# Kernel optimization log

Hardware: AMD Instinct MI355X
Metric: run time of the kernel (lower is better)

## Reference

```python
import jax, jax.numpy as jnp
import numpy as np

B, N, T_FULL, T, KS, FEAT = 32, 360, 512, 64, 8, 8
NLAYERS = 3   # DCGRU layers
GLAYERS = 4   # bidirectional GRU layers in GruKRegion


def _gru_layer(x, Wih, Whh, bih, bhh, reverse):
    # x: [M, Tg, in] -> [M, Tg, H]; PyTorch GRU gate order (r, z, n)
    M = x.shape[0]
    Hh = Whh.shape[1]
    xp = jnp.einsum('mti,gi->mtg', x, Wih) + bih  # precompute input projections
    if reverse:
        xp = xp[:, ::-1]

    def step(h, xg):
        gh = jnp.einsum('mh,gh->mg', h, Whh) + bhh
        xr, xz, xn = jnp.split(xg, 3, -1)
        hr, hz, hn = jnp.split(gh, 3, -1)
        r = jax.nn.sigmoid(xr + hr)
        z = jax.nn.sigmoid(xz + hz)
        n = jnp.tanh(xn + r * hn)
        hnew = (1.0 - z) * n + z * h
        return hnew, hnew

    _, hs = jax.lax.scan(step, jnp.zeros((M, Hh), x.dtype), jnp.swapaxes(xp, 0, 1))
    hs = jnp.swapaxes(hs, 0, 1)
    if reverse:
        hs = hs[:, ::-1]
    return hs


def _dcgru_cell(x, h, adj, gw, gb, cw, cb):
    # x, h: [B, N] (rnn_units = 1); adj: [B, N, N]; max_diffusion_step = 2
    def gconv(inp, st, W, bias):
        x0 = jnp.stack([inp, st], axis=-1)                     # [B,N,2]
        x1 = jnp.einsum('bnm,bmc->bnc', adj, x0)
        x2 = 2.0 * jnp.einsum('bnm,bmc->bnc', adj, x1) - x0    # Chebyshev recurrence
        # torch layout: [B,N,C,num_matrices] flattened channel-major
        xc = jnp.stack([x0, x1, x2], axis=-1).reshape(x0.shape[0], N, 6)
        return jnp.einsum('bnf,fo->bno', xc, W) + bias

    gates = jax.nn.sigmoid(gconv(x, h, gw, gb))                # [B,N,2]
    r, u = gates[..., 0], gates[..., 1]
    c = jnp.tanh(gconv(x, r * h, cw, cb)[..., 0])
    return u * h + (1.0 - u) * c


def _forward(full_seq, reconstruct_seq, node_feas, temperature,
             g0wih, g0whh, g0bih, g0bhh, gwih, gwhh, gbih, gbhh,
             l1w, l1b, l2w, l2b,
             enc_gw, enc_gb, enc_cw, enc_cb,
             dec_gw, dec_gb, dec_cw, dec_cb, proj_w, proj_b):
    b, n, tfull = full_seq.shape
    # ---- GruKRegion feature extractor ----
    x = full_seq.reshape(b * n, tfull // KS, KS)
    out = jnp.concatenate(
        [_gru_layer(x, g0wih[0], g0whh[0], g0bih[0], g0bhh[0], False),
         _gru_layer(x, g0wih[1], g0whh[1], g0bih[1], g0bhh[1], True)], axis=-1)
    for l in range(GLAYERS - 1):
        out = jnp.concatenate(
            [_gru_layer(out, gwih[l, 0], gwhh[l, 0], gbih[l, 0], gbhh[l, 0], False),
             _gru_layer(out, gwih[l, 1], gwhh[l, 1], gbih[l, 1], gbhh[l, 1], True)], axis=-1)
    feat = out[:, -1, :].reshape(b, n, 2 * KS)
    feat = jax.nn.leaky_relu(jnp.einsum('bnf,of->bno', feat, l1w) + l1b, 0.2)
    feat = jnp.einsum('bnf,of->bno', feat, l2w) + l2b          # [B,N,FEAT]
    # ---- Embed2GraphByProduct ----
    logits = jnp.einsum('bjk,bpk->bjp', feat, feat)            # [B,N,N]
    # ---- hard gumbel softmax ----
    U = jax.random.uniform(jax.random.key(42), logits.shape, logits.dtype)
    g = -jnp.log(-jnp.log(U + 1e-10) + 1e-10)
    y_soft = jax.nn.softmax((logits + g) / temperature, axis=-1)
    y_hard = jax.nn.one_hot(jnp.argmax(y_soft, -1), n, dtype=y_soft.dtype)
    adj = y_soft + jax.lax.stop_gradient(y_hard - y_soft)
    adj = jnp.where(jnp.eye(n, dtype=bool), 0.0, adj)          # zero diagonal
    # (original computes a random-walk matrix then discards it; skipped)
    # ---- encoder: scan over time, 3 stacked DCGRU layers ----
    seq = jnp.transpose(reconstruct_seq, (2, 0, 1))            # [T,B,N]

    def enc_step(hid, xt):
        o = xt
        new = []
        for l in range(NLAYERS):
            hnew = _dcgru_cell(o, hid[l], adj, enc_gw[l], enc_gb[l], enc_cw[l], enc_cb[l])
            new.append(hnew)
            o = hnew
        return jnp.stack(new), None

    hid, _ = jax.lax.scan(enc_step, jnp.zeros((NLAYERS, b, n), seq.dtype), seq)

    def dec_step(carry, _):
        hidc, inp = carry
        o = inp
        new = []
        for l in range(NLAYERS):
            hnew = _dcgru_cell(o, hidc[l], adj, dec_gw[l], dec_gb[l], dec_cw[l], dec_cb[l])
            new.append(hnew)
            o = hnew
        proj = o * proj_w[0, 0] + proj_b[0]                    # Linear(1,1)
        return (jnp.stack(new), proj), proj

    _, outs = jax.lax.scan(dec_step, (hid, jnp.zeros((b, n), seq.dtype)), None, length=T)
    return jnp.transpose(outs, (1, 2, 0))                      # [B,N,T]


def setup_inputs():
    key = jax.random.key(0)
    ks = jax.random.split(key, 24)
    s = 0.2
    p = lambda k, sh: jax.random.normal(k, sh, jnp.float32) * s
    return dict(
        full_seq=jax.random.normal(ks[0], (B, N, T_FULL), jnp.float32),
        reconstruct_seq=jax.random.normal(ks[1], (B, N, T), jnp.float32),
        node_feas=jax.random.normal(ks[2], (B, N, KS), jnp.float32),
        temperature=jnp.ones((), jnp.float32),
        g0wih=p(ks[3], (2, 3 * KS, KS)), g0whh=p(ks[4], (2, 3 * KS, KS)),
        g0bih=p(ks[5], (2, 3 * KS)), g0bhh=p(ks[6], (2, 3 * KS)),
        gwih=p(ks[7], (GLAYERS - 1, 2, 3 * KS, 2 * KS)),
        gwhh=p(ks[8], (GLAYERS - 1, 2, 3 * KS, KS)),
        gbih=p(ks[9], (GLAYERS - 1, 2, 3 * KS)), gbhh=p(ks[10], (GLAYERS - 1, 2, 3 * KS)),
        l1w=p(ks[11], (KS, 2 * KS)), l1b=p(ks[12], (KS,)),
        l2w=p(ks[13], (FEAT, KS)), l2b=p(ks[14], (FEAT,)),
        enc_gw=p(ks[15], (NLAYERS, 6, 2)), enc_gb=jnp.ones((NLAYERS, 2), jnp.float32),
        enc_cw=p(ks[16], (NLAYERS, 6, 1)), enc_cb=jnp.zeros((NLAYERS, 1), jnp.float32),
        dec_gw=p(ks[17], (NLAYERS, 6, 2)), dec_gb=jnp.ones((NLAYERS, 2), jnp.float32),
        dec_cw=p(ks[18], (NLAYERS, 6, 1)), dec_cb=jnp.zeros((NLAYERS, 1), jnp.float32),
        proj_w=p(ks[19], (1, 1)), proj_b=jnp.zeros((1,), jnp.float32),
    )


def reference(full_seq, reconstruct_seq, node_feas, temperature,
              g0wih, g0whh, g0bih, g0bhh, gwih, gwhh, gbih, gbhh,
              l1w, l1b, l2w, l2b,
              enc_gw, enc_gb, enc_cw, enc_cb,
              dec_gw, dec_gb, dec_cw, dec_cb, proj_w, proj_b):
    return _forward(full_seq, reconstruct_seq, node_feas, temperature,
                    g0wih, g0whh, g0bih, g0bhh, gwih, gwhh, gbih, gbhh,
                    l1w, l1b, l2w, l2b,
                    enc_gw, enc_gb, enc_cw, enc_cb,
                    dec_gw, dec_gb, dec_cw, dec_cb, proj_w, proj_b)
```

## Files before the change

kernel.cpp:

```cpp
#include <hip/hip_runtime.h>
#include <math.h>

#define M_SEQ 11520
#define NNODE 360
#define NB    32
#define TT    64

__device__ __forceinline__ float fsigd(float x)  { return 1.0f / (1.0f + __expf(-x)); }
__device__ __forceinline__ float ftanhd(float x) { return 1.0f - 2.0f / (__expf(2.0f * x) + 1.0f); }

__device__ __forceinline__ void lds_barrier()
{
    asm volatile("s_waitcnt lgkmcnt(0)" ::: "memory");
    __builtin_amdgcn_sched_barrier(0);
    __builtin_amdgcn_s_barrier();
    __builtin_amdgcn_sched_barrier(0);
}

__device__ __forceinline__ unsigned rotl32(unsigned x, int n) { return (x << n) | (x >> (32 - n)); }

__device__ __forceinline__ void tf2x32(unsigned& x0, unsigned& x1)
{
    const unsigned k0 = 0u, k1 = 42u, k2 = 0u ^ 42u ^ 0x1BD11BDAu;
    x0 += k0; x1 += k1;
#define R4(a,b,c,d) \
    x0 += x1; x1 = rotl32(x1,a); x1 ^= x0; \
    x0 += x1; x1 = rotl32(x1,b); x1 ^= x0; \
    x0 += x1; x1 = rotl32(x1,c); x1 ^= x0; \
    x0 += x1; x1 = rotl32(x1,d); x1 ^= x0;
    R4(13,15,26,6)   x0 += k1; x1 += k2 + 1u;
    R4(17,29,16,24)  x0 += k2; x1 += k0 + 2u;
    R4(13,15,26,6)   x0 += k0; x1 += k1 + 3u;
    R4(17,29,16,24)  x0 += k1; x1 += k2 + 4u;
    R4(13,15,26,6)   x0 += k2; x1 += k0 + 5u;
#undef R4
}

__device__ __forceinline__ float jax_uniform(unsigned idx)
{
    unsigned x0 = 0u, x1 = idx;
    tf2x32(x0, x1);
    unsigned bits = x0 ^ x1;
    return __uint_as_float((bits >> 9) | 0x3f800000u) - 1.0f;
}

template<int K>
__device__ __forceinline__ void swz_gather(float h, float* __restrict__ hb)
{
    hb[K] = __int_as_float(
        __builtin_amdgcn_ds_swizzle(__float_as_int(h), (K << 5) | 0x18));
    if constexpr (K < 7)
        swz_gather<K + 1>(h, hb);
}

template<int I>
__device__ __forceinline__ void ldx(float* __restrict__ xv, const float* __restrict__ p)
{
    const float4* p4 = reinterpret_cast<const float4*>(p);
#pragma unroll
    for (int q = 0; q < I / 4; ++q) {
        float4 f = p4[q];
        xv[4*q] = f.x; xv[4*q+1] = f.y; xv[4*q+2] = f.z; xv[4*q+3] = f.w;
    }
}

template<int I>
__device__ __forceinline__ void xgates(const float* __restrict__ xv,
    const float* wx0, const float* wx1, const float* wx2,
    float bx0, float bx1, float bx2, float& xr, float& xz, float& xn)
{
    xr = bx0; xz = bx1; xn = bx2;
#pragma unroll
    for (int k = 0; k < I; ++k) {
        xr += xv[k] * wx0[k];
        xz += xv[k] * wx1[k];
        xn += xv[k] * wx2[k];
    }
}

__device__ __forceinline__ float hstep(float h, float xr, float xz, float xn,
    const float* w0, const float* w1, const float* w2,
    float bh0, float bh1, float bh2)
{
    float hb[8];
    swz_gather<0>(h, hb);
    float gh0 = bh0, gh1 = bh1, gh2 = bh2;
#pragma unroll
    for (int k = 0; k < 8; ++k) {
        gh0 += hb[k] * w0[k];
        gh1 += hb[k] * w1[k];
        gh2 += hb[k] * w2[k];
    }
    float r  = fsigd(xr + gh0);
    float z  = fsigd(xz + gh1);
    float nn = ftanhd(xn + r * gh2);
    return (1.f - z) * nn + z * h;
}

template<int I, bool LASTONLY>
__global__ __launch_bounds__(256) void gru_fused(
    const float* __restrict__ x,
    const float* __restrict__ wih,
    const float* __restrict__ whh,
    const float* __restrict__ bih,
    const float* __restrict__ bhh,
    float* __restrict__ out)
{
    const int tid = blockIdx.x * 256 + threadIdx.x;
    const int j   = tid & 7;
    const int md  = tid >> 3;
    if (md >= M_SEQ * 2) return;
    const int m = md >> 1, dir = md & 1;

    float wx0[I], wx1[I], wx2[I];
    const float* WI = wih + dir * 24 * I;
#pragma unroll
    for (int k = 0; k < I; ++k) {
        wx0[k] = WI[j * I + k];
        wx1[k] = WI[(8 + j) * I + k];
        wx2[k] = WI[(16 + j) * I + k];
    }
    float w0[8], w1[8], w2[8];
    const float* WH = whh + dir * 192;
#pragma unroll
    for (int k = 0; k < 8; ++k) {
        w0[k] = WH[j * 8 + k];
        w1[k] = WH[(8 + j) * 8 + k];
        w2[k] = WH[(16 + j) * 8 + k];
    }
    const float bx0 = bih[dir*24 + j], bx1 = bih[dir*24 + 8 + j], bx2 = bih[dir*24 + 16 + j];
    const float bh0 = bhh[dir*24 + j], bh1 = bhh[dir*24 + 8 + j], bh2 = bhh[dir*24 + 16 + j];

    const float* xm = x + (size_t)m * TT * I;
    float* om = out + (size_t)m * TT * 16 + dir * 8 + j;

    const int tstep = dir ? -1 : 1;
    const int tbase = dir ? TT - 1 : 0;

    float h = 0.f;
    float xva[I], xvb[I];
    ldx<I>(xva, xm + (tbase) * I);
    ldx<I>(xvb, xm + (tbase + tstep) * I);
    float cr, cz, cn;
    xgates<I>(xva, wx0, wx1, wx2, bx0, bx1, bx2, cr, cz, cn);

    for (int tt = 0; tt < TT; tt += 2) {
        const int t0 = tbase + tstep * tt;
        const int t1 = t0 + tstep;
        if (tt + 2 < TT) ldx<I>(xva, xm + (t0 + 2 * tstep) * I);
        float nr, nz, nn;
        xgates<I>(xvb, wx0, wx1, wx2, bx0, bx1, bx2, nr, nz, nn);
        h = hstep(h, cr, cz, cn, w0, w1, w2, bh0, bh1, bh2);
        if (!LASTONLY || t0 == TT - 1) om[t0 * 16] = h;
        if (tt + 3 < TT) ldx<I>(xvb, xm + (t0 + 3 * tstep) * I);
        h = hstep(h, nr, nz, nn, w0, w1, w2, bh0, bh1, bh2);
        if (!LASTONLY || t1 == TT - 1) om[t1 * 16] = h;
        xgates<I>(xva, wx0, wx1, wx2, bx0, bx1, bx2, cr, cz, cn);
    }
}

__global__ void feat_kernel(const float* __restrict__ gout,
                            const float* __restrict__ l1w, const float* __restrict__ l1b,
                            const float* __restrict__ l2w, const float* __restrict__ l2b,
                            float* __restrict__ feat)
{
    int m = blockIdx.x * blockDim.x + threadIdx.x;
    if (m >= M_SEQ) return;
    const float* xp = gout + (size_t)m * TT * 16 + (TT - 1) * 16;
    float xv[16];
#pragma unroll
    for (int i = 0; i < 16; ++i) xv[i] = xp[i];
    float h1[8];
#pragma unroll
    for (int o = 0; o < 8; ++o) {
        float a = 0.f;
#pragma unroll
        for (int f = 0; f < 16; ++f) a += xv[f] * l1w[o * 16 + f];
        a += l1b[o];
        h1[o] = (a >= 0.f) ? a : 0.2f * a;
    }
#pragma unroll
    for (int o = 0; o < 8; ++o) {
        float a = 0.f;
#pragma unroll
        for (int f = 0; f < 8; ++f) a += h1[f] * l2w[o * 8 + f];
        feat[(size_t)m * 8 + o] = a + l2b[o];
    }
}

__global__ void adj_kernel(const float* __restrict__ feat,
                           const float* __restrict__ tptr,
                           int* __restrict__ colp, float* __restrict__ vp)
{
    const int gw   = (blockIdx.x * blockDim.x + threadIdx.x) >> 6;
    const int lane = threadIdx.x & 63;
    if (gw >= NB * NNODE) return;
    const int b = gw / NNODE;
    const int n = gw - b * NNODE;
    const float T = tptr[0];
    const float* fb = feat + (size_t)b * NNODE * 8;
    float fn[8];
#pragma unroll
    for (int k = 0; k < 8; ++k) fn[k] = fb[(size_t)n * 8 + k];

    float sv[6];
    float mval = -3.0e38f; int midx = 1 << 30;
#pragma unroll
    for (int s = 0; s < 6; ++s) {
        int p = s * 64 + lane;
        float xs = -3.0e38f;
        if (p < NNODE) {
            const float* fp = fb + (size_t)p * 8;
            float d = 0.f;
#pragma unroll
            for (int k = 0; k < 8; ++k) d += fn[k] * fp[k];
            unsigned idx = (unsigned)gw * 360u + (unsigned)p;
            float u   = jax_uniform(idx);
            float gum = -logf(-logf(u + 1e-10f) + 1e-10f);
            xs = (d + gum) / T;
            if (xs > mval) { mval = xs; midx = p; }
        }
        sv[s] = xs;
    }
    for (int off = 32; off > 0; off >>= 1) {
        float ov = __shfl_xor(mval, off);
        int   oi = __shfl_xor(midx, off);
        if (ov > mval || (ov == mval && oi < midx)) { mval = ov; midx = oi; }
    }
    float ssum = 0.f;
#pragma unroll
    for (int s = 0; s < 6; ++s) {
        int p = s * 64 + lane;
        if (p < NNODE) ssum += expf(sv[s] - mval);
    }
    for (int off = 32; off > 0; off >>= 1) ssum += __shfl_xor(ssum, off);
    if (lane == 0) {
        float ys = 1.0f / ssum;
        float v  = ys + (1.0f - ys);
        if (midx == n) v = 0.0f;
        colp[gw] = midx;
        vp[gw]   = v;
    }
}

__device__ __forceinline__ void dc_layer(
    bool comp,
    float o_own, float oa, float ob,
    float& hn, float ha, float hb,
    float v, float vv, int c1, int c2, bool act, int n,
    const float* __restrict__ W, float bgr, float bgu,
    const float* __restrict__ C, float cb,
    float* __restrict__ s_rh)
{
    float f1 = 0.f, f2 = 0.f, f4 = 0.f, f5 = 0.f, rh = 0.f;
    if (comp) {
        f1 = v * oa; f2 = vv * ob - o_own;
        f4 = v * ha; f5 = vv * hb - hn;
        float r = fsigd(o_own*W[0] + f1*W[2] + f2*W[4] + hn*W[6] + f4*W[8] + f5*W[10] + bgr);
        rh = r * hn;
        if (act) s_rh[n] = rh;
    }
    lds_barrier();
    if (comp) {
        float rha = s_rh[c1], rhb = s_rh[c2];
        float u  = fsigd(o_own*W[1] + f1*W[3] + f2*W[5] + hn*W[7] + f4*W[9] + f5*W[11] + bgu);
        float cnd = ftanhd(o_own*C[0] + f1*C[1] + f2*C[2] + rh*C[3]
                           + (v*rha)*C[4] + (vv*rhb - rh)*C[5] + cb);
        hn = u * hn + (1.f - u) * cnd;
    }
}

__global__ __launch_bounds__(768, 1) void decode_kernel(
    const float* __restrict__ rec,
    const int*   __restrict__ colp, const float* __restrict__ vp,
    const float* __restrict__ egw, const float* __restrict__ egb,
    const float* __restrict__ ecw, const float* __restrict__ ecb,
    const float* __restrict__ dgw, const float* __restrict__ dgb,
    const float* __restrict__ dcw, const float* __restrict__ dcb,
    const float* __restrict__ pw,  const float* __restrict__ pb,
    float* __restrict__ outp)
{
    __shared__ float s_h[2][3][NNODE];
    __shared__ float s_xe[2][NNODE];
    __shared__ float s_r1[2][NNODE];
    __shared__ float s_u1[2][NNODE];
    __shared__ float s_c1[2][NNODE];
    __shared__ float s_rh0[NNODE];
    __shared__ float s_rh2[NNODE];
    __shared__ float s_o[NNODE];
    __shared__ float s_rhd[NNODE];
    __shared__ float s_v[NNODE];
    __shared__ int   s_c[NNODE];

    const int  b    = blockIdx.x;
    const int  tid  = threadIdx.x;
    const bool isB  = tid >= 384;
    const bool isA  = !isB;
    const int  node = isB ? tid - 384 : tid;
    const bool actN = node < NNODE;

    const float* recb = rec + ((size_t)b * NNODE + node) * TT;

    float o_own = 0.f, xq1 = 0.f;
    if (isA && actN) {
        s_c[node] = colp[b * NNODE + node];
        s_v[node] = vp[b * NNODE + node];
        o_own = recb[0];
        xq1   = recb[1];
        s_xe[0][node] = o_own;
#pragma unroll
        for (int l = 0; l < 3; ++l) { s_h[0][l][node] = 0.f; s_h[1][l][node] = 0.f; }
    }
    __syncthreads();

    int c1 = 0, c2 = 0;
    float v = 0.f, vv = 0.f;
    if (actN) {
        c1 = s_c[node];
        c2 = s_c[c1];
        v  = s_v[node];
        vv = 2.f * v * s_v[c1];
    }
    const float projw = pw[0], projb = pb[0];

    float Wg[36], Bg[6], Wc[18], Cb[3];
#pragma unroll
    for (int k = 0; k < 36; ++k) Wg[k] = egw[k];
#pragma unroll
    for (int k = 0; k < 6;  ++k) Bg[k] = egb[k];
#pragma unroll
    for (int k = 0; k < 18; ++k) Wc[k] = ecw[k];
#pragma unroll
    for (int k = 0; k < 3;  ++k) Cb[k] = ecb[k];

    float h0r = 0.f, h1r = 0.f, h2r = 0.f;

    for (int k = 0; k <= TT; ++k) {
        const int  pk = k & 1, qk = pk ^ 1;
        const bool aAct = isA && actN && (k < TT);
        const bool bAct = isB && actN && (k >= 1);
        float nx2 = 0.f;
        if (aAct && k + 2 < TT) nx2 = recb[k + 2];

        float fA1=0.f, fA2=0.f, fA4=0.f, fA5=0.f, rhA=0.f;
        if (isA) {
            float xa  = s_xe[pk][c1],   xb  = s_xe[pk][c2];
            float h0a = s_h[pk][0][c1], h0b = s_h[pk][0][c2];
            fA1 = v * xa;  fA2 = vv * xb - o_own;
            fA4 = v * h0a; fA5 = vv * h0b - h0r;
            float rA = fsigd(o_own*Wg[0] + fA1*Wg[2] + fA2*Wg[4] + h0r*Wg[6]
                             + fA4*Wg[8] + fA5*Wg[10] + Bg[0]);
            rhA = rA * h0r;
            if (aAct) s_rh0[node] = rhA;
        } else {
            float rh1o = s_r1[pk][node];
            float rh1a = s_r1[pk][c1], rh1b = s_r1[pk][c2];
            float u1v  = s_u1[pk][node], cp1v = s_c1[pk][node];
            float cnd1 = ftanhd(cp1v + rh1o*Wc[9] + (v*rh1a)*Wc[10]
                                + (vv*rh1b - rh1o)*Wc[11] + Cb[1]);
            if (bAct) { h1r = u1v * h1r + (1.f - u1v) * cnd1; s_h[qk][1][node] = h1r; }
        }
        lds_barrier();

        float fB1=0.f, fB2=0.f, fB4=0.f, fB5=0.f, rhB=0.f;
        if (isA) {
            float rh0a = s_rh0[c1], rh0b = s_rh0[c2];
            float uA = fsigd(o_own*Wg[1] + fA1*Wg[3] + fA2*Wg[5] + h0r*Wg[7]
                             + fA4*Wg[9] + fA5*Wg[11] + Bg[1]);
            float cndA = ftanhd(o_own*Wc[0] + fA1*Wc[1] + fA2*Wc[2] + rhA*Wc[3]
                                + (v*rh0a)*Wc[4] + (vv*rh0b - rhA)*Wc[5] + Cb[0]);
            if (aAct) {
                h0r = uA * h0r + (1.f - uA) * cndA;
                s_h[qk][0][node] = h0r;
                s_xe[qk][node]   = xq1;
            }
        } else {
            float o2a = s_h[qk][1][c1], o2b = s_h[qk][1][c2];
            float h2a = s_h[pk][2][c1], h2b = s_h[pk][2][c2];
            fB1 = v * o2a; fB2 = vv * o2b - h1r;
            fB4 = v * h2a; fB5 = vv * h2b - h2r;
            float rB = fsigd(h1r*Wg[24] + fB1*Wg[26] + fB2*Wg[28] + h2r*Wg[30]
                             + fB4*Wg[32] + fB5*Wg[34] + Bg[4]);
            rhB = rB * h2r;
            if (bAct) s_rh2[node] = rhB;
        }
        lds_barrier();

        if (isA) {
            float o1a = s_h[qk][0][c1], o1b = s_h[qk][0][c2];
            float h1own = s_h[qk][1][node];
            float h1a = s_h[qk][1][c1], h1b = s_h[qk][1][c2];
            float fC1 = v * o1a, fC2 = vv * o1b - h0r;
            float fC4 = v * h1a, fC5 = vv * h1b - h1own;
            float r1 = fsigd(h0r*Wg[12] + fC1*Wg[14] + fC2*Wg[16] + h1own*Wg[18]
                             + fC4*Wg[20] + fC5*Wg[22] + Bg[2]);
            float u1 = fsigd(h0r*Wg[13] + fC1*Wg[15] + fC2*Wg[17] + h1own*Wg[19]
                             + fC4*Wg[21] + fC5*Wg[23] + Bg[3]);
            float cp1 = h0r*Wc[6] + fC1*Wc[7] + fC2*Wc[8];
            if (aAct) { s_r1[qk][node] = r1 * h1own; s_u1[qk][node] = u1; s_c1[qk][node] = cp1; }
        } else {
            float rh2a = s_rh2[c1], rh2b = s_rh2[c2];
            float u2 = fsigd(h1r*Wg[25] + fB1*Wg[27] + fB2*Wg[29] + h2r*Wg[31]
                             + fB4*Wg[33] + fB5*Wg[35] + Bg[5]);
            float cnd2 = ftanhd(h1r*Wc[12] + fB1*Wc[13] + fB2*Wc[14] + rhB*Wc[15]
                                + (v*rh2a)*Wc[16] + (vv*rh2b - rhB)*Wc[17] + Cb[2]);
            if (bAct) { h2r = u2 * h2r + (1.f - u2) * cnd2; s_h[qk][2][node] = h2r; }
        }
        lds_barrier();
        if (isA) { o_own = xq1; xq1 = nx2; }
    }

    if (tid < NNODE) {
        s_h[0][1][tid] = s_h[1][1][tid];
        s_h[0][2][tid] = s_h[1][2][tid];
        s_xe[0][tid]   = 0.f;
    }
    __syncthreads();

    const bool actd = (isA && actN);
    const int  nd   = actN ? node : 0;
    float hreg[3];
    hreg[0] = h0r;
    hreg[1] = s_h[0][1][nd];
    hreg[2] = s_h[0][2][nd];

#pragma unroll
    for (int k = 0; k < 36; ++k) Wg[k] = dgw[k];
#pragma unroll
    for (int k = 0; k < 6;  ++k) Bg[k] = dgb[k];
#pragma unroll
    for (int k = 0; k < 18; ++k) Wc[k] = dcw[k];
#pragma unroll
    for (int k = 0; k < 3;  ++k) Cb[k] = dcb[k];

    float dinp = 0.f;
    int p = 0;
    for (int t = 0; t < TT; ++t) {
        float xa=0.f, xb=0.f;
        float h0a=0.f,h0b=0.f,h1a=0.f,h1b=0.f,h2a=0.f,h2b=0.f;
        if (isA) {
            xa  = s_xe[p][c1];     xb  = s_xe[p][c2];
            h0a = s_h[p][0][c1];   h0b = s_h[p][0][c2];
            h1a = s_h[p][1][c1];   h1b = s_h[p][1][c2];
            h2a = s_h[p][2][c1];   h2b = s_h[p][2][c2];
        }
        const int q = p ^ 1;
        dc_layer(isA, dinp, xa, xb, hreg[0], h0a, h0b, v, vv, c1, c2, actd, node,
                 Wg, Bg[0], Bg[1], Wc, Cb[0], s_rhd);
        if (actd) { s_h[q][0][node] = hreg[0]; s_o[node] = hreg[0]; }
        lds_barrier();
        float oa=0.f, ob=0.f;
        if (isA) { oa = s_o[c1]; ob = s_o[c2]; }
        dc_layer(isA, hreg[0], oa, ob, hreg[1], h1a, h1b, v, vv, c1, c2, actd, node,
                 Wg + 12, Bg[2], Bg[3], Wc + 6, Cb[1], s_rhd);
        if (actd) { s_h[q][1][node] = hreg[1]; s_o[node] = hreg[1]; }
        lds_barrier();
        if (isA) { oa = s_o[c1]; ob = s_o[c2]; }
        dc_layer(isA, hreg[1], oa, ob, hreg[2], h2a, h2b, v, vv, c1, c2, actd, node,
                 Wg + 24, Bg[4], Bg[5], Wc + 12, Cb[2], s_rhd);
        float proj = hreg[2] * projw + projb;
        if (actd) {
            s_h[q][2][node] = hreg[2];
            s_xe[q][node]   = proj;
            outp[((size_t)b * NNODE + node) * TT + t] = proj;
        }
        lds_barrier();
        dinp = proj; p = q;
    }
}

extern "C" void kernel_launch(void* const* d_in, const int* in_sizes, int n_in,
                              void* d_out, int out_size, void* d_ws, size_t ws_size,
                              hipStream_t stream)
{
    (void)in_sizes; (void)n_in; (void)out_size; (void)ws_size;
    const float* full_seq = (const float*)d_in[0];
    const float* rec_seq  = (const float*)d_in[1];
    const float* temp     = (const float*)d_in[3];
    const float* g0wih    = (const float*)d_in[4];
    const float* g0whh    = (const float*)d_in[5];
    const float* g0bih    = (const float*)d_in[6];
    const float* g0bhh    = (const float*)d_in[7];
    const float* gwih     = (const float*)d_in[8];
    const float* gwhh     = (const float*)d_in[9];
    const float* gbih     = (const float*)d_in[10];
    const float* gbhh     = (const float*)d_in[11];
    const float* l1w      = (const float*)d_in[12];
    const float* l1b      = (const float*)d_in[13];
    const float* l2w      = (const float*)d_in[14];
    const float* l2b      = (const float*)d_in[15];
    const float* enc_gw   = (const float*)d_in[16];
    const float* enc_gb   = (const float*)d_in[17];
    const float* enc_cw   = (const float*)d_in[18];
    const float* enc_cb   = (const float*)d_in[19];
    const float* dec_gw   = (const float*)d_in[20];
    const float* dec_gb   = (const float*)d_in[21];
    const float* dec_cw   = (const float*)d_in[22];
    const float* dec_cb   = (const float*)d_in[23];
    const float* proj_w   = (const float*)d_in[24];
    const float* proj_b   = (const float*)d_in[25];
    float* outp = (float*)d_out;

    float* ws   = (float*)d_ws;
    float* feat = ws;
    float* vbuf = feat + (size_t)M_SEQ * 8;
    int*   cbuf = (int*)(vbuf + M_SEQ);
    float* bufA = (float*)(cbuf + M_SEQ);
    float* bufB = bufA + (size_t)M_SEQ * TT * 16;

    const int ggru = (M_SEQ * 2 * 8) / 256;
    gru_fused<8,false><<<ggru, 256, 0, stream>>>(full_seq, g0wih, g0whh, g0bih, g0bhh, bufA);
    gru_fused<16,false><<<ggru, 256, 0, stream>>>(bufA, gwih + 0 * 768, gwhh + 0 * 384,
                                                  gbih + 0 * 48, gbhh + 0 * 48, bufB);
    gru_fused<16,false><<<ggru, 256, 0, stream>>>(bufB, gwih + 1 * 768, gwhh + 1 * 384,
                                                  gbih + 1 * 48, gbhh + 1 * 48, bufA);
    gru_fused<16,true><<<ggru, 256, 0, stream>>>(bufA, gwih + 2 * 768, gwhh + 2 * 384,
                                                 gbih + 2 * 48, gbhh + 2 * 48, bufB);
    feat_kernel<<<M_SEQ / 256, 256, 0, stream>>>(bufB, l1w, l1b, l2w, l2b, feat);
    adj_kernel<<<(NB * NNODE) / 4, 256, 0, stream>>>(feat, temp, cbuf, vbuf);
    decode_kernel<<<NB, 768, 0, stream>>>(rec_seq, cbuf, vbuf,
                                          enc_gw, enc_gb, enc_cw, enc_cb,
                                          dec_gw, dec_gb, dec_cw, dec_cb,
                                          proj_w, proj_b, outp);
}
```

Baseline: 513.9 us.

## Split GRU input projection across two lanes for 16-wide layers

```diff
diff --git a/kernel.cpp b/kernel.cpp
--- a/kernel.cpp
+++ b/kernel.cpp
@@ -156,6 +156,73 @@
         h = hstep(h, nr, nz, nn, w0, w1, w2, bh0, bh1, bh2);
         if (!LASTONLY || t1 == TT - 1) om[t1 * 16] = h;
         xgates<I>(xva, wx0, wx1, wx2, bx0, bx1, bx2, cr, cz, cn);
+    }
+}
+
+template<bool LASTONLY>
+__global__ __launch_bounds__(256) void gru_split(
+    const float* __restrict__ x,
+    const float* __restrict__ wih,
+    const float* __restrict__ whh,
+    const float* __restrict__ bih,
+    const float* __restrict__ bhh,
+    float* __restrict__ out)
+{
+    const int tid  = blockIdx.x * 256 + threadIdx.x;
+    const int j    = tid & 7;
+    const int half = (tid >> 3) & 1;
+    const int dir  = (tid >> 4) & 1;
+    const int m    = tid >> 5;
+
+    float wx0[8], wx1[8], wx2[8];
+    const float* WI = wih + dir * 24 * 16 + half * 8;
+#pragma unroll
+    for (int k = 0; k < 8; ++k) {
+        wx0[k] = WI[j * 16 + k];
+        wx1[k] = WI[(8 + j) * 16 + k];
+        wx2[k] = WI[(16 + j) * 16 + k];
+    }
+    float w0[8], w1[8], w2[8];
+    const float* WH = whh + dir * 192;
+#pragma unroll
+    for (int k = 0; k < 8; ++k) {
+        w0[k] = WH[j * 8 + k];
+        w1[k] = WH[(8 + j) * 8 + k];
+        w2[k] = WH[(16 + j) * 8 + k];
+    }
+    const float bx0 = half ? 0.f : bih[dir*24 + j];
+    const float bx1 = half ? 0.f : bih[dir*24 + 8 + j];
+    const float bx2 = half ? 0.f : bih[dir*24 + 16 + j];
+    const float bh0 = bhh[dir*24 + j], bh1 = bhh[dir*24 + 8 + j], bh2 = bhh[dir*24 + 16 + j];
+
+    const float* xm = x + (size_t)m * TT * 16 + half * 8;
+    float* om = out + (size_t)m * TT * 16 + dir * 8 + j;
+
+    const int tstep = dir ? -1 : 1;
+    const int tbase = dir ? TT - 1 : 0;
+
+    float h = 0.f;
+    float xva[8], xvb[8];
+    ldx<8>(xva, xm + (tbase) * 16);
+    ldx<8>(xvb, xm + (tbase + tstep) * 16);
+    float cr, cz, cn;
+    xgates<8>(xva, wx0, wx1, wx2, bx0, bx1, bx2, cr, cz, cn);
+    cr += __shfl_xor(cr, 8); cz += __shfl_xor(cz, 8); cn += __shfl_xor(cn, 8);
+
+    for (int tt = 0; tt < TT; tt += 2) {
+        const int t0 = tbase + tstep * tt;
+        const int t1 = t0 + tstep;
+        if (tt + 2 < TT) ldx<8>(xva, xm + (t0 + 2 * tstep) * 16);
+        float nr, nz, nn;
+        xgates<8>(xvb, wx0, wx1, wx2, bx0, bx1, bx2, nr, nz, nn);
+        nr += __shfl_xor(nr, 8); nz += __shfl_xor(nz, 8); nn += __shfl_xor(nn, 8);
+        h = hstep(h, cr, cz, cn, w0, w1, w2, bh0, bh1, bh2);
+        if (half == 0 && (!LASTONLY || t0 == TT - 1)) om[t0 * 16] = h;
+        if (tt + 3 < TT) ldx<8>(xvb, xm + (t0 + 3 * tstep) * 16);
+        h = hstep(h, nr, nz, nn, w0, w1, w2, bh0, bh1, bh2);
+        if (half == 0 && (!LASTONLY || t1 == TT - 1)) om[t1 * 16] = h;
+        xgates<8>(xva, wx0, wx1, wx2, bx0, bx1, bx2, cr, cz, cn);
+        cr += __shfl_xor(cr, 8); cz += __shfl_xor(cz, 8); cn += __shfl_xor(cn, 8);
     }
 }
 
@@ -508,14 +575,15 @@
     float* bufA = (float*)(cbuf + M_SEQ);
     float* bufB = bufA + (size_t)M_SEQ * TT * 16;
 
-    const int ggru = (M_SEQ * 2 * 8) / 256;
+    const int ggru  = (M_SEQ * 2 * 8) / 256;
+    const int gsplit = (M_SEQ * 32) / 256;
     gru_fused<8,false><<<ggru, 256, 0, stream>>>(full_seq, g0wih, g0whh, g0bih, g0bhh, bufA);
-    gru_fused<16,false><<<ggru, 256, 0, stream>>>(bufA, gwih + 0 * 768, gwhh + 0 * 384,
-                                                  gbih + 0 * 48, gbhh + 0 * 48, bufB);
-    gru_fused<16,false><<<ggru, 256, 0, stream>>>(bufB, gwih + 1 * 768, gwhh + 1 * 384,
-                                                  gbih + 1 * 48, gbhh + 1 * 48, bufA);
-    gru_fused<16,true><<<ggru, 256, 0, stream>>>(bufA, gwih + 2 * 768, gwhh + 2 * 384,
-                                                 gbih + 2 * 48, gbhh + 2 * 48, bufB);
+    gru_split<false><<<gsplit, 256, 0, stream>>>(bufA, gwih + 0 * 768, gwhh + 0 * 384,
+                                                 gbih + 0 * 48, gbhh + 0 * 48, bufB);
+    gru_split<false><<<gsplit, 256, 0, stream>>>(bufB, gwih + 1 * 768, gwhh + 1 * 384,
+                                                 gbih + 1 * 48, gbhh + 1 * 48, bufA);
+    gru_split<true><<<gsplit, 256, 0, stream>>>(bufA, gwih + 2 * 768, gwhh + 2 * 384,
+                                                gbih + 2 * 48, gbhh + 2 * 48, bufB);
     feat_kernel<<<M_SEQ / 256, 256, 0, stream>>>(bufB, l1w, l1b, l2w, l2b, feat);
     adj_kernel<<<(NB * NNODE) / 4, 256, 0, stream>>>(feat, temp, cbuf, vbuf);
     decode_kernel<<<NB, 768, 0, stream>>>(rec_seq, cbuf, vbuf,
```

Result: slower. 579.4 us (+12.7%).
